# Kernel tuning notes

Measured on AMD Instinct MI355X. Metric: run time of the kernel, lower is better.

The kernel has to match this reference:

```python
import jax, jax.numpy as jnp
import numpy as np

B0 = 0.01       # baseline threshold (Yin et al. ALIF)
BETA = 1.8      # adaptation coupling strength
SG_GAMMA = 0.5  # surrogate gradient scale
SG_LENS = 0.5   # surrogate gradient width

@jax.custom_vjp
def spike(v):
    return (v > 0.0).astype(v.dtype)

def _spike_fwd(v):
    return spike(v), v

def _spike_bwd(v, g):
    sg = SG_GAMMA * jnp.exp(-0.5 * (v / SG_LENS) ** 2) / (jnp.sqrt(2.0 * jnp.pi) * SG_LENS)
    return (g * sg,)

spike.defvjp(_spike_fwd, _spike_bwd)

def alif_forward(x, W_h, tau_mem, tau_adp, W_o, tau_out):
    # x: [T, B, I]; W_h: [H, I+H]; W_o: [O, H]
    T, B, _ = x.shape
    H = W_h.shape[0]
    O = W_o.shape[0]
    alpha = jnp.exp(-1.0 / tau_mem)    # [H] membrane decay
    rho = jnp.exp(-1.0 / tau_adp)      # [H] adaptation decay
    alpha_o = jnp.exp(-1.0 / tau_out)  # [O] output leaky-integrator decay
    z0 = jnp.zeros((B, H), x.dtype)
    u0 = jnp.zeros((B, H), x.dtype)
    a0 = jnp.zeros((B, H), x.dtype)
    ou0 = jnp.zeros((B, O), x.dtype)

    def step(carry, x_t):
        z, u, a, ou = carry
        cur = jnp.concatenate([x_t, z], axis=1) @ W_h.T   # [B, H]
        a = rho * a + (1.0 - rho) * z                     # adaptation from previous spike
        theta = B0 + BETA * a                             # adaptive threshold
        u = alpha * u + (1.0 - alpha) * cur - z * theta   # leaky integrate + soft reset
        z = spike(u - theta)                              # heaviside w/ surrogate grad
        ou = alpha_o * ou + (1.0 - alpha_o) * (z @ W_o.T) # LI readout
        return (z, u, a, ou), (ou, jnp.sum(z))

    (zT, uT, aT, ouT), (outputs, spikes) = jax.lax.scan(step, (z0, u0, a0, ou0), x)
    return outputs, (zT, uT, aT, ouT), jnp.sum(spikes)

def setup_inputs() -> dict:
    key = jax.random.key(0)
    ks = jax.random.split(key, 6)
    T, B, I, H, O = 250, 256, 700, 1024, 20
    x = jax.random.normal(ks[0], (T, B, I), jnp.float32)
    W_h = jax.random.normal(ks[1], (H, I + H), jnp.float32) / np.sqrt(I + H).astype(np.float32)
    tau_mem = 20.0 + 5.0 * jax.random.normal(ks[2], (H,), jnp.float32)
    tau_adp = 20.0 + 5.0 * jax.random.normal(ks[3], (H,), jnp.float32)
    W_o = jax.random.normal(ks[4], (O, H), jnp.float32) / np.sqrt(H).astype(np.float32)
    tau_out = 20.0 + 5.0 * jax.random.normal(ks[5], (O,), jnp.float32)
    return {"x": x, "W_h": W_h, "tau_mem": tau_mem, "tau_adp": tau_adp, "W_o": W_o, "tau_out": tau_out}

def reference(x, W_h, tau_mem, tau_adp, W_o, tau_out):
    outputs, (zT, uT, aT, ouT), num_spikes = alif_forward(x, W_h, tau_mem, tau_adp, W_o, tau_out)
    # matches torch forward: (outputs, ((hidden_z, hidden_u, hidden_a), out_u), num_spikes)
    return (outputs, zT, uT, aT, ouT, num_spikes)
```

## Files before the change

### kernel.cpp

```cpp
#include <hip/hip_runtime.h>

#define T_STEPS 250
#define BATCH   256
#define IN_DIM  700
#define HID     1024
#define W_LD    1724
#define OUT_DIM 20
#define KP      704
#define NKT     (KP / 32)
#define CHUNK_T 50

typedef __attribute__((ext_vector_type(8))) short     bf16x8;
typedef __attribute__((ext_vector_type(8))) unsigned short u16x8;
typedef __attribute__((ext_vector_type(4))) float     f32x4;
typedef unsigned long long u64;

__device__ inline unsigned short f2bf(float f) {
    unsigned int u = __float_as_uint(f);
    unsigned int r = u + 0x7FFFu + ((u >> 16) & 1u);
    return (unsigned short)(r >> 16);
}
__device__ inline float bf2f(unsigned short w) {
    return __uint_as_float(((unsigned int)w) << 16);
}

__global__ __launch_bounds__(256)
void trans_whh_bf16(const float* __restrict__ W_h, unsigned short* __restrict__ WhhT) {
    __shared__ float tile[32][33];
    const int bx = blockIdx.x * 32;
    const int by = blockIdx.y * 32;
    const int tx = threadIdx.x, ty = threadIdx.y;
#pragma unroll
    for (int i = 0; i < 32; i += 8)
        tile[ty + i][tx] = W_h[(size_t)(bx + ty + i) * W_LD + IN_DIM + by + tx];
    __syncthreads();
#pragma unroll
    for (int i = 0; i < 32; i += 8)
        WhhT[(size_t)(by + ty + i) * HID + bx + tx] = f2bf(tile[tx][ty + i]);
}

__global__ __launch_bounds__(256)
void trans_wo(const float* __restrict__ Wo, float* __restrict__ WoT) {
    const int h = blockIdx.x * 256 + threadIdx.x;
    if (h >= HID) return;
#pragma unroll
    for (int o = 0; o < OUT_DIM; ++o)
        WoT[(size_t)h * OUT_DIM + o] = Wo[(size_t)o * HID + h];
}

__global__ __launch_bounds__(256)
void pack_w_bf16(const float* __restrict__ W_h, unsigned short* __restrict__ Wp) {
    const int total = HID * (KP / 4);
    for (int idx = blockIdx.x * blockDim.x + threadIdx.x; idx < total;
         idx += gridDim.x * blockDim.x) {
        const int r = idx / (KP / 4);
        const int c = idx - r * (KP / 4);
        ushort4 o = make_ushort4(0, 0, 0, 0);
        if (c < IN_DIM / 4) {
            float4 v = *(const float4*)(W_h + (size_t)r * W_LD + c * 4);
            o = make_ushort4(f2bf(v.x), f2bf(v.y), f2bf(v.z), f2bf(v.w));
        }
        ((ushort4*)Wp)[(size_t)r * (KP / 4) + c] = o;
    }
}

__device__ __forceinline__ u16x8 ldx8(const float* __restrict__ row, int k) {
    u16x8 r;
    if (k <= IN_DIM - 8) {
        float4 a = *(const float4*)(row + k);
        float4 b = *(const float4*)(row + k + 4);
        r[0] = f2bf(a.x); r[1] = f2bf(a.y); r[2] = f2bf(a.z); r[3] = f2bf(a.w);
        r[4] = f2bf(b.x); r[5] = f2bf(b.y); r[6] = f2bf(b.z); r[7] = f2bf(b.w);
    } else if (k < IN_DIM) {
        float4 a = *(const float4*)(row + k);
        r[0] = f2bf(a.x); r[1] = f2bf(a.y); r[2] = f2bf(a.z); r[3] = f2bf(a.w);
        r[4] = 0; r[5] = 0; r[6] = 0; r[7] = 0;
    } else {
        r = (u16x8){0,0,0,0,0,0,0,0};
    }
    return r;
}

__device__ __forceinline__
void gemm_body(char* smem, const float* __restrict__ X,
               const unsigned short* __restrict__ B, unsigned short* __restrict__ C,
               int bm, int bn) {
    unsigned short* lA = (unsigned short*)smem;
    unsigned short* lB = (unsigned short*)(smem + 8192);
    const int tid  = threadIdx.x;
    const int wid  = tid >> 6, lane = tid & 63;
    const int wr   = wid >> 1, wc = wid & 1;

    const int srow = tid >> 2;
    const int skq  = (tid & 3) * 8;

    const int wb0 = (srow * 64 + (tid & 3) * 16) ^ ((srow & 7) << 4);
    const int wb1 = ((srow + 64) * 64 + (tid & 3) * 16) ^ ((srow & 7) << 4);

    const float* xr0 = X + (size_t)(bm + srow) * IN_DIM;
    const float* xr1 = X + (size_t)(bm + srow + 64) * IN_DIM;
    const unsigned short* pb = B + (size_t)(bn + srow) * KP + skq;

    u16x8 ra0, ra1, rb0, rb1;
    auto ldg = [&](int k0) {
        ra0 = ldx8(xr0, k0 + skq);
        ra1 = ldx8(xr1, k0 + skq);
        rb0 = *(const u16x8*)(pb + k0);
        rb1 = *(const u16x8*)(pb + (size_t)64 * KP + k0);
    };

    const int arow = wr * 64 + (lane & 15);
    const int brow = wc * 64 + (lane & 15);
    const int fq   = (lane >> 4) * 16;

    f32x4 acc[4][4];
#pragma unroll
    for (int m = 0; m < 4; ++m)
#pragma unroll
        for (int n = 0; n < 4; ++n) acc[m][n] = (f32x4){0.f, 0.f, 0.f, 0.f};

    ldg(0);
    for (int kt = 0; kt < NKT; ++kt) {
        *(u16x8*)((char*)lA + wb0) = ra0;
        *(u16x8*)((char*)lA + wb1) = ra1;
        *(u16x8*)((char*)lB + wb0) = rb0;
        *(u16x8*)((char*)lB + wb1) = rb1;
        __syncthreads();
        if (kt + 1 < NKT) ldg((kt + 1) * 32);
        bf16x8 af[4], bf[4];
#pragma unroll
        for (int m = 0; m < 4; ++m) {
            const int row = arow + m * 16;
            af[m] = *(const bf16x8*)((const char*)lA + ((row * 64 + fq) ^ ((row & 7) << 4)));
        }
#pragma unroll
        for (int n = 0; n < 4; ++n) {
            const int row = brow + n * 16;
            bf[n] = *(const bf16x8*)((const char*)lB + ((row * 64 + fq) ^ ((row & 7) << 4)));
        }
#pragma unroll
        for (int m = 0; m < 4; ++m)
#pragma unroll
            for (int n = 0; n < 4; ++n)
                acc[m][n] = __builtin_amdgcn_mfma_f32_16x16x32_bf16(af[m], bf[n], acc[m][n], 0, 0, 0);
        __syncthreads();
    }
#pragma unroll
    for (int m = 0; m < 4; ++m)
#pragma unroll
        for (int r = 0; r < 4; ++r) {
            unsigned short* cp = C + (size_t)(bm + wr * 64 + m * 16 + (lane >> 4) * 4 + r) * HID
                               + bn + wc * 64 + (lane & 15);
#pragma unroll
            for (int n = 0; n < 4; ++n)
                __builtin_nontemporal_store(f2bf(acc[m][n][r]), cp + n * 16);
        }
}

#define G_LDIDX(JJ, g)                                                        \
    {                                                                         \
        const int base_ = lo + (g) * 4;                                       \
        JJ[0] = (base_ + 0 < hi) ? (int)lst[base_ + 0] : 1024;                \
        JJ[1] = (base_ + 1 < hi) ? (int)lst[base_ + 1] : 1024;                \
        JJ[2] = (base_ + 2 < hi) ? (int)lst[base_ + 2] : 1024;                \
        JJ[3] = (base_ + 3 < hi) ? (int)lst[base_ + 3] : 1024;                \
    }

#define G_ISSUE(WB, JJ)                                                       \
    {                                                                         \
        _Pragma("unroll")                                                     \
        for (int q_ = 0; q_ < 4; ++q_) {                                      \
            const unsigned int* p_ = Wrow32 + ((size_t)JJ[q_] << 9);          \
            WB[q_ * 2 + 0] = *(const uint4*)p_;                               \
            WB[q_ * 2 + 1] = *(const uint4*)(p_ + 4);                         \
        }                                                                     \
    }

#define G_ACCUM(WB)                                                           \
    {                                                                         \
        _Pragma("unroll")                                                     \
        for (int q_ = 0; q_ < 4; ++q_) {                                      \
            const uint4 w0_ = WB[q_ * 2 + 0];                                 \
            const uint4 w1_ = WB[q_ * 2 + 1];                                 \
            pacc[0][0] += __uint_as_float(w0_.x << 16);                       \
            pacc[0][1] += __uint_as_float(w0_.x & 0xFFFF0000u);               \
            pacc[0][2] += __uint_as_float(w0_.y << 16);                       \
            pacc[0][3] += __uint_as_float(w0_.y & 0xFFFF0000u);               \
            pacc[1][0] += __uint_as_float(w0_.z << 16);                       \
            pacc[1][1] += __uint_as_float(w0_.z & 0xFFFF0000u);               \
            pacc[1][2] += __uint_as_float(w0_.w << 16);                       \
            pacc[1][3] += __uint_as_float(w0_.w & 0xFFFF0000u);               \
            pacc[2][0] += __uint_as_float(w1_.x << 16);                       \
            pacc[2][1] += __uint_as_float(w1_.x & 0xFFFF0000u);               \
            pacc[2][2] += __uint_as_float(w1_.y << 16);                       \
            pacc[2][3] += __uint_as_float(w1_.y & 0xFFFF0000u);               \
            pacc[3][0] += __uint_as_float(w1_.z << 16);                       \
            pacc[3][1] += __uint_as_float(w1_.z & 0xFFFF0000u);               \
            pacc[3][2] += __uint_as_float(w1_.w << 16);                       \
            pacc[3][3] += __uint_as_float(w1_.w & 0xFFFF0000u);               \
        }                                                                     \
    }

__device__ __forceinline__
void scan_body(char* smem, const unsigned short* __restrict__ CUR,
               const unsigned short* __restrict__ WhhT,
               const float* __restrict__ tau_mem, const float* __restrict__ tau_adp,
               float* __restrict__ zS, float* __restrict__ uS, float* __restrict__ aS,
               float* __restrict__ spkS, unsigned short* __restrict__ masks16,
               int t0, int tc) {
    const int tid  = threadIdx.x;
    const int wv   = tid >> 6;
    const int lane = tid & 63;
    const int b    = blockIdx.x;
    const int h0   = lane * 16;

    unsigned short (*s_idx)[2][1040] = (unsigned short (*)[2][1040])smem;
    f32x4 (*s_part)[4][64]           = (f32x4 (*)[4][64])(smem + 16640);

    float u[16], a[16], alpha[16], rho[16];
#pragma unroll
    for (int q = 0; q < 4; ++q) {
        f32x4 uu = *(const f32x4*)(uS + (size_t)b * HID + h0 + q * 4);
        f32x4 aa = *(const f32x4*)(aS + (size_t)b * HID + h0 + q * 4);
        f32x4 tm = *(const f32x4*)(tau_mem + h0 + q * 4);
        f32x4 ta = *(const f32x4*)(tau_adp + h0 + q * 4);
#pragma unroll
        for (int k = 0; k < 4; ++k) {
            u[q * 4 + k] = uu[k];  a[q * 4 + k] = aa[k];
            alpha[q * 4 + k] = expf(-1.f / tm[k]);
            rho[q * 4 + k]   = expf(-1.f / ta[k]);
        }
    }
    unsigned int zb = 0;
#pragma unroll
    for (int q = 0; q < 4; ++q) {
        f32x4 zz = *(const f32x4*)(zS + (size_t)b * HID + h0 + q * 4);
#pragma unroll
        for (int k = 0; k < 4; ++k)
            if (zz[k] > 0.5f) zb |= (1u << (q * 4 + k));
    }

    int n;
    {
        const int cnt = __popc(zb);
        int incl = cnt;
#pragma unroll
        for (int d = 1; d < 64; d <<= 1) {
            int v = __shfl_up(incl, d, 64);
            if (lane >= d) incl += v;
        }
        int off = incl - cnt;
        unsigned int tmp = zb;
        while (tmp) {
            const int k = __ffs(tmp) - 1;
            tmp &= tmp - 1;
            s_idx[wv][0][off++] = (unsigned short)(h0 + k);
        }
        n = __shfl(incl, 63, 64);
    }

    const unsigned int* Wrow32 = (const unsigned int*)WhhT + (h0 >> 1);
    float xc[16];
    {
        const unsigned short* p = CUR + (size_t)b * HID + h0;
        u16x8 v0 = *(const u16x8*)p;
        u16x8 v1 = *(const u16x8*)(p + 8);
#pragma unroll
        for (int k = 0; k < 8; ++k) {
            xc[k]     = bf2f((unsigned short)v0[k]);
            xc[k + 8] = bf2f((unsigned short)v1[k]);
        }
    }
    __syncthreads();

    int cur = 0;
    int wspk = 0;
    for (int tt = 0; tt < tc; ++tt) {
        float xn[16];
        {
            const int tn = (tt + 1 < tc) ? tt + 1 : tt;
            const unsigned short* p = CUR + ((size_t)tn * BATCH + b) * HID + h0;
            u16x8 v0 = *(const u16x8*)p;
            u16x8 v1 = *(const u16x8*)(p + 8);
#pragma unroll
            for (int k = 0; k < 8; ++k) {
                xn[k]     = bf2f((unsigned short)v0[k]);
                xn[k + 8] = bf2f((unsigned short)v1[k]);
            }
        }

        f32x4 pacc[4];
#pragma unroll
        for (int q = 0; q < 4; ++q) pacc[q] = (f32x4){0.f, 0.f, 0.f, 0.f};

        if (n > 0) {
            const unsigned short* lst = s_idx[wv][cur];
            const int lo = (n * wv) >> 2;
            const int hi = (n * (wv + 1)) >> 2;
            const int m = hi - lo;
            if (m > 0) {
                const int ng = (m + 3) >> 2;
                int  jA[4], jB[4];
                uint4 wA[8], wB[8];
                G_LDIDX(jA, 0);
                G_ISSUE(wA, jA);
                int g = 0;
                while (true) {
                    if (g + 1 < ng) { G_LDIDX(jB, g + 1); G_ISSUE(wB, jB); }
                    G_ACCUM(wA);
                    if (++g >= ng) break;
                    if (g + 1 < ng) { G_LDIDX(jA, g + 1); G_ISSUE(wA, jA); }
                    G_ACCUM(wB);
                    if (++g >= ng) break;
                }
            }
            s_part[wv][0][lane] = pacc[0];
            s_part[wv][1][lane] = pacc[1];
            s_part[wv][2][lane] = pacc[2];
            s_part[wv][3][lane] = pacc[3];
            __syncthreads();
#pragma unroll
            for (int q = 0; q < 4; ++q) {
                f32x4 r0 = s_part[0][q][lane];
                f32x4 r1 = s_part[1][q][lane];
                f32x4 r2 = s_part[2][q][lane];
                f32x4 r3 = s_part[3][q][lane];
                pacc[q] = ((r0 + r1) + r2) + r3;
            }
        }

        unsigned int znb = 0;
#pragma unroll
        for (int k = 0; k < 16; ++k) {
            const float rec = pacc[k >> 2][k & 3];
            const float z   = (zb >> k) & 1 ? 1.f : 0.f;
            const float omr = 1.f - rho[k];
            const float oma = 1.f - alpha[k];
            a[k] = rho[k] * a[k] + omr * z;
            const float th = 0.01f + 1.8f * a[k];
            u[k] = alpha[k] * u[k] + oma * (xc[k] + rec) - z * th;
            if (u[k] - th > 0.f) znb |= (1u << k);
        }
        zb = znb;
        wspk += __popc(zb);
        if (wv == 0)
            masks16[((size_t)(t0 + tt) * BATCH + b) * 64 + lane] = (unsigned short)zb;

        {
            const int cnt = __popc(zb);
            int incl = cnt;
#pragma unroll
            for (int d = 1; d < 64; d <<= 1) {
                int v = __shfl_up(incl, d, 64);
                if (lane >= d) incl += v;
            }
            int off = incl - cnt;
            unsigned int tmp = zb;
            while (tmp) {
                const int k = __ffs(tmp) - 1;
                tmp &= tmp - 1;
                s_idx[wv][cur ^ 1][off++] = (unsigned short)(h0 + k);
            }
            n = __shfl(incl, 63, 64);
        }
#pragma unroll
        for (int k = 0; k < 16; ++k) xc[k] = xn[k];
        __syncthreads();
        cur ^= 1;
    }

    if (wv == 0) {
#pragma unroll
        for (int k = 0; k < 16; ++k) {
            zS[(size_t)b * HID + h0 + k] = (zb >> k) & 1 ? 1.f : 0.f;
            uS[(size_t)b * HID + h0 + k] = u[k];
            aS[(size_t)b * HID + h0 + k] = a[k];
        }
#pragma unroll
        for (int d = 32; d > 0; d >>= 1) wspk += __shfl_down(wspk, d, 64);
        if (lane == 0) atomicAdd(spkS, (float)wspk);
    }
}

__global__ __launch_bounds__(256, 2)
void fused_scan_gemm(const unsigned short* __restrict__ CUR,
                     const unsigned short* __restrict__ WhhT,
                     const float* __restrict__ tau_mem, const float* __restrict__ tau_adp,
                     float* __restrict__ zS, float* __restrict__ uS, float* __restrict__ aS,
                     float* __restrict__ spkS, unsigned short* __restrict__ masks16,
                     int t0, int tc,
                     const float* __restrict__ Xn, const unsigned short* __restrict__ Wp,
                     unsigned short* __restrict__ CURn) {
    __shared__ __align__(16) char smem[33024];
    if ((int)blockIdx.x < BATCH) {
        scan_body(smem, CUR, WhhT, tau_mem, tau_adp, zS, uS, aS, spkS,
                  masks16, t0, tc);
    } else {
        const int gb = (int)blockIdx.x - BATCH;
        gemm_body(smem, Xn, Wp, CURn, (gb >> 3) * 128, (gb & 7) * 128);
    }
}

__global__ __launch_bounds__(256)
void gemm_pro(const float* __restrict__ X, const unsigned short* __restrict__ Wp,
              unsigned short* __restrict__ C) {
    __shared__ __align__(16) char smem[16384];
    const int gb = (int)blockIdx.x;
    gemm_body(smem, X, Wp, C, (gb >> 3) * 128, (gb & 7) * 128);
}

__global__ __launch_bounds__(256)
void readout_y(const u64* __restrict__ masks, const float* __restrict__ WoT,
               float* __restrict__ y, int npairs) {
    const int pr   = blockIdx.x * 4 + (threadIdx.x >> 6);
    const int lane = threadIdx.x & 63;
    if (pr >= npairs) return;
    const u64* mp = masks + (size_t)pr * 16;
    float acc = 0.f;
#pragma unroll 4
    for (int w = 0; w < 16; ++w) {
        u64 m = mp[w];
        while (m) {
            const int j = __ffsll((unsigned long long)m) - 1;
            m &= m - 1;
            if (lane < OUT_DIM) acc += WoT[(size_t)(w * 64 + j) * OUT_DIM + lane];
        }
    }
    if (lane < OUT_DIM) y[(size_t)pr * OUT_DIM + lane] = acc;
}

__global__ __launch_bounds__(256)
void ewa_out(const float* __restrict__ y, const float* __restrict__ tau_out,
             float* __restrict__ outputs, float* __restrict__ ouS) {
    const int idx = blockIdx.x * 256 + threadIdx.x;
    if (idx >= BATCH * OUT_DIM) return;
    const int o = idx % OUT_DIM;
    const float ao = expf(-1.f / tau_out[o]);
    float ou = ouS[idx];
    for (int t = 0; t < T_STEPS; ++t) {
        const float v = y[(size_t)t * BATCH * OUT_DIM + idx];
        ou = ao * ou + (1.f - ao) * v;
        outputs[(size_t)t * BATCH * OUT_DIM + idx] = ou;
    }
    ouS[idx] = ou;
}

extern "C" void kernel_launch(void* const* d_in, const int* in_sizes, int n_in,
                              void* d_out, int out_size, void* d_ws, size_t ws_size,
                              hipStream_t stream) {
    (void)in_sizes; (void)n_in; (void)out_size; (void)ws_size;
    const float* x       = (const float*)d_in[0];
    const float* W_h     = (const float*)d_in[1];
    const float* tau_mem = (const float*)d_in[2];
    const float* tau_adp = (const float*)d_in[3];
    const float* W_o     = (const float*)d_in[4];
    const float* tau_out = (const float*)d_in[5];

    float* out     = (float*)d_out;
    float* outputs = out;
    float* zS  = out + (size_t)T_STEPS * BATCH * OUT_DIM;
    float* uS  = zS + (size_t)BATCH * HID;
    float* aS  = uS + (size_t)BATCH * HID;
    float* ouS = aS + (size_t)BATCH * HID;
    float* spk = ouS + (size_t)BATCH * OUT_DIM;

    char* w = (char*)d_ws;
    unsigned short* WhhT = (unsigned short*)w; w += (size_t)(HID + 1) * HID * 2;
    unsigned short* Wp   = (unsigned short*)w; w += (size_t)HID * KP * 2;
    float*          WoT  = (float*)w;          w += (size_t)HID * OUT_DIM * 4;
    unsigned short* masks16 = (unsigned short*)w; w += (size_t)T_STEPS * BATCH * 128;
    float*          yBuf = (float*)w;          w += (size_t)T_STEPS * BATCH * OUT_DIM * 4;
    unsigned short* CUR_A = (unsigned short*)w; w += (size_t)CHUNK_T * BATCH * HID * 2;
    unsigned short* CUR_B = (unsigned short*)w;

    const int mB    = CHUNK_T * BATCH / 128;
    const int gemmG = mB * (HID / 128);

    hipMemsetAsync(zS, 0,
                   ((size_t)3 * BATCH * HID + BATCH * OUT_DIM + 1) * sizeof(float),
                   stream);
    hipMemsetAsync(WhhT + (size_t)HID * HID, 0, HID * sizeof(unsigned short), stream);
    trans_whh_bf16<<<dim3(32, 32), dim3(32, 8), 0, stream>>>(W_h, WhhT);
    pack_w_bf16<<<512, 256, 0, stream>>>(W_h, Wp);
    trans_wo<<<4, 256, 0, stream>>>(W_o, WoT);

    gemm_pro<<<gemmG, 256, 0, stream>>>(x, Wp, CUR_A);

    const int nChunks = T_STEPS / CHUNK_T;
    for (int c = 0; c < nChunks; ++c) {
        const int t0 = c * CHUNK_T;
        unsigned short* CURc = (c & 1) ? CUR_B : CUR_A;
        unsigned short* CURn = (c & 1) ? CUR_A : CUR_B;
        const bool more = (c + 1 < nChunks);
        const int grid = BATCH + (more ? gemmG : 0);
        fused_scan_gemm<<<grid, 256, 0, stream>>>(
            CURc, WhhT, tau_mem, tau_adp, zS, uS, aS, spk, masks16,
            t0, CHUNK_T,
            x + (size_t)(t0 + CHUNK_T) * BATCH * IN_DIM, Wp, CURn);
    }

    const int npairs = T_STEPS * BATCH;
    readout_y<<<(npairs + 3) / 4, 256, 0, stream>>>((const u64*)masks16, WoT, yBuf, npairs);
    ewa_out<<<(BATCH * OUT_DIM + 255) / 256, 256, 0, stream>>>(yBuf, tau_out, outputs, ouS);
}
```

Before: 981.5 us.

## Overlap spike readout with next scan chunk and use uneven chunk sizes

The readout of spike masks for the previous chunk now runs as extra blocks inside the fused scan/GEMM launch, instead of one large readout kernel after the whole scan. Chunks are resized to 30,55,55,55,55 so the serial prologue GEMM is shorter. Only the last chunk's readout stays after the loop. Readout blocks compete with the scan blocks for CU resources, which could slow the critical-path scan, and larger later chunks raise the GEMM share per launch.

```diff
diff --git a/kernel.cpp b/kernel.cpp
--- a/kernel.cpp
+++ b/kernel.cpp
@@ -8,7 +8,7 @@
 #define OUT_DIM 20
 #define KP      704
 #define NKT     (KP / 32)
-#define CHUNK_T 50
+#define MAXCT   55
 
 typedef __attribute__((ext_vector_type(8))) short     bf16x8;
 typedef __attribute__((ext_vector_type(8))) unsigned short u16x8;
@@ -382,39 +382,10 @@
     }
 }
 
-__global__ __launch_bounds__(256, 2)
-void fused_scan_gemm(const unsigned short* __restrict__ CUR,
-                     const unsigned short* __restrict__ WhhT,
-                     const float* __restrict__ tau_mem, const float* __restrict__ tau_adp,
-                     float* __restrict__ zS, float* __restrict__ uS, float* __restrict__ aS,
-                     float* __restrict__ spkS, unsigned short* __restrict__ masks16,
-                     int t0, int tc,
-                     const float* __restrict__ Xn, const unsigned short* __restrict__ Wp,
-                     unsigned short* __restrict__ CURn) {
-    __shared__ __align__(16) char smem[33024];
-    if ((int)blockIdx.x < BATCH) {
-        scan_body(smem, CUR, WhhT, tau_mem, tau_adp, zS, uS, aS, spkS,
-                  masks16, t0, tc);
-    } else {
-        const int gb = (int)blockIdx.x - BATCH;
-        gemm_body(smem, Xn, Wp, CURn, (gb >> 3) * 128, (gb & 7) * 128);
-    }
-}
-
-__global__ __launch_bounds__(256)
-void gemm_pro(const float* __restrict__ X, const unsigned short* __restrict__ Wp,
-              unsigned short* __restrict__ C) {
-    __shared__ __align__(16) char smem[16384];
-    const int gb = (int)blockIdx.x;
-    gemm_body(smem, X, Wp, C, (gb >> 3) * 128, (gb & 7) * 128);
-}
-
-__global__ __launch_bounds__(256)
-void readout_y(const u64* __restrict__ masks, const float* __restrict__ WoT,
-               float* __restrict__ y, int npairs) {
-    const int pr   = blockIdx.x * 4 + (threadIdx.x >> 6);
+__device__ __forceinline__
+void readout_body(const u64* __restrict__ masks, const float* __restrict__ WoT,
+                  float* __restrict__ y, int pr) {
     const int lane = threadIdx.x & 63;
-    if (pr >= npairs) return;
     const u64* mp = masks + (size_t)pr * 16;
     float acc = 0.f;
 #pragma unroll 4
@@ -427,6 +398,47 @@
         }
     }
     if (lane < OUT_DIM) y[(size_t)pr * OUT_DIM + lane] = acc;
+}
+
+__global__ __launch_bounds__(256, 2)
+void fused_scan_gemm(const unsigned short* __restrict__ CUR,
+                     const unsigned short* __restrict__ WhhT,
+                     const float* __restrict__ tau_mem, const float* __restrict__ tau_adp,
+                     float* __restrict__ zS, float* __restrict__ uS, float* __restrict__ aS,
+                     float* __restrict__ spkS, unsigned short* __restrict__ masks16,
+                     int t0, int tc,
+                     const float* __restrict__ Xn, const unsigned short* __restrict__ Wp,
+                     unsigned short* __restrict__ CURn, int gemmG,
+                     const u64* __restrict__ masksAll, const float* __restrict__ WoT,
+                     float* __restrict__ yBuf, int pr0, int prN) {
+    __shared__ __align__(16) char smem[33024];
+    const int bid = (int)blockIdx.x;
+    if (bid < BATCH) {
+        scan_body(smem, CUR, WhhT, tau_mem, tau_adp, zS, uS, aS, spkS,
+                  masks16, t0, tc);
+    } else if (bid < BATCH + gemmG) {
+        const int gb = bid - BATCH;
+        gemm_body(smem, Xn, Wp, CURn, (gb >> 3) * 128, (gb & 7) * 128);
+    } else {
+        const int rb = bid - BATCH - gemmG;
+        const int pi = rb * 4 + ((int)threadIdx.x >> 6);
+        if (pi < prN) readout_body(masksAll, WoT, yBuf, pr0 + pi);
+    }
+}
+
+__global__ __launch_bounds__(256)
+void gemm_pro(const float* __restrict__ X, const unsigned short* __restrict__ Wp,
+              unsigned short* __restrict__ C) {
+    __shared__ __align__(16) char smem[16384];
+    const int gb = (int)blockIdx.x;
+    gemm_body(smem, X, Wp, C, (gb >> 3) * 128, (gb & 7) * 128);
+}
+
+__global__ __launch_bounds__(256)
+void readout_y(const u64* __restrict__ masks, const float* __restrict__ WoT,
+               float* __restrict__ y, int pr0, int npairs) {
+    const int pi = (int)blockIdx.x * 4 + ((int)threadIdx.x >> 6);
+    if (pi < npairs) readout_body(masks, WoT, y, pr0 + pi);
 }
 
 __global__ __launch_bounds__(256)
@@ -470,11 +482,13 @@
     float*          WoT  = (float*)w;          w += (size_t)HID * OUT_DIM * 4;
     unsigned short* masks16 = (unsigned short*)w; w += (size_t)T_STEPS * BATCH * 128;
     float*          yBuf = (float*)w;          w += (size_t)T_STEPS * BATCH * OUT_DIM * 4;
-    unsigned short* CUR_A = (unsigned short*)w; w += (size_t)CHUNK_T * BATCH * HID * 2;
+    unsigned short* CUR_A = (unsigned short*)w; w += (size_t)MAXCT * BATCH * HID * 2;
     unsigned short* CUR_B = (unsigned short*)w;
 
-    const int mB    = CHUNK_T * BATCH / 128;
-    const int gemmG = mB * (HID / 128);
+    const int tcArr[5] = {30, 55, 55, 55, 55};
+    int t0Arr[5];
+    t0Arr[0] = 0;
+    for (int c = 1; c < 5; ++c) t0Arr[c] = t0Arr[c - 1] + tcArr[c - 1];
 
     hipMemsetAsync(zS, 0,
                    ((size_t)3 * BATCH * HID + BATCH * OUT_DIM + 1) * sizeof(float),
@@ -484,22 +498,28 @@
     pack_w_bf16<<<512, 256, 0, stream>>>(W_h, Wp);
     trans_wo<<<4, 256, 0, stream>>>(W_o, WoT);
 
-    gemm_pro<<<gemmG, 256, 0, stream>>>(x, Wp, CUR_A);
-
-    const int nChunks = T_STEPS / CHUNK_T;
-    for (int c = 0; c < nChunks; ++c) {
-        const int t0 = c * CHUNK_T;
+    gemm_pro<<<2 * tcArr[0] * 8, 256, 0, stream>>>(x, Wp, CUR_A);
+
+    for (int c = 0; c < 5; ++c) {
+        const int t0 = t0Arr[c];
+        const int tc = tcArr[c];
         unsigned short* CURc = (c & 1) ? CUR_B : CUR_A;
         unsigned short* CURn = (c & 1) ? CUR_A : CUR_B;
-        const bool more = (c + 1 < nChunks);
-        const int grid = BATCH + (more ? gemmG : 0);
-        fused_scan_gemm<<<grid, 256, 0, stream>>>(
+        const int gemmG = (c + 1 < 5) ? 2 * tcArr[c + 1] * 8 : 0;
+        const int pr0   = (c > 0) ? t0Arr[c - 1] * BATCH : 0;
+        const int prN   = (c > 0) ? tcArr[c - 1] * BATCH : 0;
+        const int roG   = (prN + 3) / 4;
+        const float* Xn = (c + 1 < 5)
+                        ? x + (size_t)t0Arr[c + 1] * BATCH * IN_DIM : x;
+        fused_scan_gemm<<<BATCH + gemmG + roG, 256, 0, stream>>>(
             CURc, WhhT, tau_mem, tau_adp, zS, uS, aS, spk, masks16,
-            t0, CHUNK_T,
-            x + (size_t)(t0 + CHUNK_T) * BATCH * IN_DIM, Wp, CURn);
-    }
-
-    const int npairs = T_STEPS * BATCH;
-    readout_y<<<(npairs + 3) / 4, 256, 0, stream>>>((const u64*)masks16, WoT, yBuf, npairs);
+            t0, tc, Xn, Wp, CURn, gemmG,
+            (const u64*)masks16, WoT, yBuf, pr0, prN);
+    }
+
+    const int pr0L = t0Arr[4] * BATCH;
+    const int prNL = tcArr[4] * BATCH;
+    readout_y<<<(prNL + 3) / 4, 256, 0, stream>>>((const u64*)masks16, WoT,
+                                                  yBuf, pr0L, prNL);
     ewa_out<<<(BATCH * OUT_DIM + 255) / 256, 256, 0, stream>>>(yBuf, tau_out, outputs, ouS);
 }
```

After: 1.001 ms. +2.0%, slower.
